# Optimization experiments

Hardware: AMD Instinct MI355X
Metric: run time of the kernel (lower is better)

The kernel has to match this reference:

```python
import jax, jax.numpy as jnp
import numpy as np

SEQ_LENS = np.array([512, 1024, 1536, 2048, 640, 896, 1280, 1792], dtype=np.int64)
T = int(SEQ_LENS.sum())          # 9728 total tokens (cu_seq_len)
D = 2048                          # hidden_size
K = 4                             # kernel_size
GH = 256                          # generator hidden = D // 8


def setup_inputs() -> dict:
    key = jax.random.key(0)
    ks = jax.random.split(key, 6)
    return {
        "x": jax.random.normal(ks[0], (T, D), dtype=jnp.float32),
        "conv_state": jax.random.normal(ks[1], (len(SEQ_LENS), D, K - 1), dtype=jnp.float32),
        "generator_input": jax.random.normal(ks[2], (T, D), dtype=jnp.float32),
        "seq_lens": jnp.asarray(SEQ_LENS),
        "w1": jax.random.normal(ks[3], (D, GH), dtype=jnp.float32) * (1.0 / np.sqrt(D)),
        "w2": jax.random.normal(ks[4], (GH, D * K), dtype=jnp.float32) * (1.0 / np.sqrt(GH)),
        "b2": jax.random.normal(ks[5], (D * K,), dtype=jnp.float32) * 0.01,
    }


def reference(x, conv_state, generator_input, seq_lens, w1, w2, b2):
    lens = np.asarray(seq_lens)              # static ragged lengths
    B = lens.shape[0]
    L = int(lens.max())
    k = conv_state.shape[2] + 1              # kernel_size
    d = x.shape[1]
    t = x.shape[0]

    # ---- kernel generator: Linear -> SiLU -> Linear(+bias), per token ----
    h = jax.nn.silu(generator_input @ w1)                    # (T, GH)
    kern = (h @ w2 + b2).reshape(t, d, k)                    # (T, D, K)

    # ---- left-pad each ragged sequence; prepend conv_state (k-1 steps) ----
    offs = np.concatenate([[0], np.cumsum(lens)])
    x_rows, k_rows = [], []
    for i in range(B):                                        # B is small & static
        xi = jnp.concatenate([conv_state[i].T, x[offs[i]:offs[i + 1]]], axis=0)  # (len_i+k-1, D)
        x_rows.append(jnp.pad(xi, ((L + k - 1 - xi.shape[0], 0), (0, 0))))
        ki = kern[offs[i]:offs[i + 1]]                        # (len_i, D, K)
        k_rows.append(jnp.pad(ki, ((L - int(lens[i]), 0), (0, 0), (0, 0))))
    x_pad = jnp.stack(x_rows)                                 # (B, L+k-1, D)
    k_pad = jnp.stack(k_rows)                                 # (B, L, D, K)

    # new conv state = last k-1 timesteps of the (state+tokens) sequence
    new_conv_state = jnp.swapaxes(x_pad[:, -(k - 1):, :], 1, 2)  # (B, D, k-1)

    # ---- causal dynamic depthwise conv: window j uses x_pad[j:j+k] ----
    out_pad = x_pad[:, 0:L, :] * k_pad[..., 0]
    for kk in range(1, k):                                    # k=4, static tiny loop
        out_pad = out_pad + x_pad[:, kk:kk + L, :] * k_pad[..., kk]  # (B, L, D)

    # ---- un-pad back to ragged layout, apply SiLU ----
    out = jnp.concatenate([out_pad[i, L - int(lens[i]):] for i in range(B)], axis=0)  # (T, D)
    return jax.nn.silu(out), new_conv_state
```

## Files before the change

### kernel.cpp

```cpp
#include <hip/hip_runtime.h>
#include <cstdint>
#include <cstddef>

typedef __attribute__((ext_vector_type(8))) short bf16x8;
typedef __attribute__((ext_vector_type(4))) unsigned short u16x4;
typedef __attribute__((ext_vector_type(4))) unsigned u32x4;
typedef __attribute__((ext_vector_type(4))) float f32x4;
typedef unsigned short u16;

#define T_TOT 9728
#define DDIM  2048
#define GHN   256
#define NSEQ  8

__device__ __constant__ int OFFS[NSEQ + 1] = {0, 512, 1536, 3072, 5120, 5760, 6656, 7936, 9728};

__device__ __forceinline__ u16 f2bf(float f) {
  union { float f; unsigned u; } v; v.f = f;
  unsigned r = v.u + 0x7FFFu + ((v.u >> 16) & 1u);
  return (u16)(r >> 16);
}
__device__ __forceinline__ float silu_f(float v) {
  return v / (1.0f + __expf(-v));
}

__device__ __forceinline__ void pin_reg(bf16x8& v) {
  u32x4& u = reinterpret_cast<u32x4&>(v);
  asm volatile("" : "+v"(u));
}

__device__ __forceinline__ void gload_lds16(const u16* src, u16* dst) {
  __builtin_amdgcn_global_load_lds(
      (__attribute__((address_space(1))) void*)src,
      (__attribute__((address_space(3))) void*)dst,
      16, 0, 0);
}

__global__ __launch_bounds__(256)
void transpose_bf16_k(const float* __restrict__ in, u16* __restrict__ out, int R, int C) {
  __shared__ float tile[64][65];
  const int c0 = blockIdx.x * 64, r0 = blockIdx.y * 64;
  const int tid = threadIdx.x;
  const int lc = tid & 63, lr = tid >> 6;
#pragma unroll
  for (int p = 0; p < 16; ++p) {
    int r = lr + p * 4;
    tile[r][lc] = in[(size_t)(r0 + r) * C + c0 + lc];
  }
  __syncthreads();
#pragma unroll
  for (int p = 0; p < 16; ++p) {
    int c = lr + p * 4;
    out[(size_t)(c0 + c) * R + r0 + lc] = f2bf(tile[lc][c]);
  }
}

__global__ __launch_bounds__(256, 4)
void gemm1_silu(const float* __restrict__ gi, const u16* __restrict__ w1T,
                u16* __restrict__ h) {
  __shared__ u16 A[2][32][72];
  const int tid = threadIdx.x;
  const int lane = tid & 63, wid = tid >> 6;
  const int l15 = lane & 15, l4 = lane >> 4;
  const int t0 = blockIdx.x * 32;
  const int nb = blockIdx.y * 128 + wid * 32;

  f32x4 acc[2][2] = {};

  const int m0 = tid >> 4, f40 = tid & 15;
  const float* g0 = gi + (size_t)(t0 + m0) * DDIM + f40 * 4;
  const float* g1 = gi + (size_t)(t0 + m0 + 16) * DDIM + f40 * 4;

  f32x4 pv0 = *reinterpret_cast<const f32x4*>(g0);
  f32x4 pv1 = *reinterpret_cast<const f32x4*>(g1);

  int p = 0;
  for (int k0 = 0; k0 < DDIM; k0 += 64) {
    u16x4 b0, b1;
    b0[0] = f2bf(pv0[0]); b0[1] = f2bf(pv0[1]); b0[2] = f2bf(pv0[2]); b0[3] = f2bf(pv0[3]);
    b1[0] = f2bf(pv1[0]); b1[1] = f2bf(pv1[1]); b1[2] = f2bf(pv1[2]); b1[3] = f2bf(pv1[3]);
    *reinterpret_cast<u16x4*>(&A[p][m0][f40 * 4]) = b0;
    *reinterpret_cast<u16x4*>(&A[p][m0 + 16][f40 * 4]) = b1;
    if (k0 + 64 < DDIM) {
      pv0 = *reinterpret_cast<const f32x4*>(g0 + k0 + 64);
      pv1 = *reinterpret_cast<const f32x4*>(g1 + k0 + 64);
    }
    __syncthreads();
#pragma unroll
    for (int ks = 0; ks < 2; ++ks) {
      bf16x8 af[2], bfr[2];
#pragma unroll
      for (int mi = 0; mi < 2; ++mi)
        af[mi] = *reinterpret_cast<const bf16x8*>(&A[p][mi * 16 + l15][ks * 32 + 8 * l4]);
#pragma unroll
      for (int ni = 0; ni < 2; ++ni)
        bfr[ni] = *reinterpret_cast<const bf16x8*>(
            &w1T[(size_t)(nb + ni * 16 + l15) * DDIM + k0 + ks * 32 + 8 * l4]);
#pragma unroll
      for (int mi = 0; mi < 2; ++mi)
#pragma unroll
        for (int ni = 0; ni < 2; ++ni)
          acc[mi][ni] = __builtin_amdgcn_mfma_f32_16x16x32_bf16(af[mi], bfr[ni], acc[mi][ni], 0, 0, 0);
    }
    p ^= 1;
  }

#pragma unroll
  for (int mi = 0; mi < 2; ++mi)
#pragma unroll
    for (int ni = 0; ni < 2; ++ni)
#pragma unroll
      for (int r = 0; r < 4; ++r) {
        float v = silu_f(acc[mi][ni][r]);
        int token = t0 + mi * 16 + l4 * 4 + r;
        int c = nb + ni * 16 + l15;
        int pos = ((((c >> 3) ^ (token & 7)) << 3) | (c & 7));
        h[(size_t)token * GHN + pos] = f2bf(v);
      }
}

__global__ __launch_bounds__(256, 2)
void gemm2_conv(const u16* __restrict__ h, const u16* __restrict__ w2T,
                const float* __restrict__ b2, const float* __restrict__ x,
                const float* __restrict__ cs, float* __restrict__ out) {
  __shared__ u16 H[2][64 * 256];
  __shared__ float Ot[64 * 33];
  const int tid = threadIdx.x;
  const int lane = tid & 63, wid = tid >> 6;
  const int l15 = lane & 15, l4 = lane >> 4;
  const int colwave = blockIdx.x * 128 + wid * 32;
  const int d0 = blockIdx.x * 32;
  const int tg = blockIdx.y;

  const int ocol = colwave + 4 * (l15 >> 1) + 2 * (l15 & 1);

  bf16x8 bw[8][2];
#pragma unroll
  for (int ks = 0; ks < 8; ++ks)
#pragma unroll
    for (int ni = 0; ni < 2; ++ni)
      bw[ks][ni] = *reinterpret_cast<const bf16x8*>(
          w2T + (size_t)(ocol + ni) * GHN + ks * 32 + l4 * 8);
#pragma unroll
  for (int ks = 0; ks < 8; ++ks)
#pragma unroll
    for (int ni = 0; ni < 2; ++ni)
      pin_reg(bw[ks][ni]);

  float b2v[2];
#pragma unroll
  for (int ni = 0; ni < 2; ++ni) b2v[ni] = b2[ocol + ni];

  const int d = (colwave >> 2) + (l15 >> 1);
  const int dloc = wid * 8 + (l15 >> 1);
  const int k0t = 2 * (l15 & 1);
  const int par = lane & 1;

  {
    const u16* hb = h + (size_t)(tg * 4) * 64 * GHN;
#pragma unroll
    for (int p = 0; p < 8; ++p)
      gload_lds16(hb + (size_t)(p * 256 + tid) * 8, &H[0][(p * 256 + tid) * 8]);
  }
  __syncthreads();

  int cur = 0;
  for (int it = 0; it < 4; ++it) {
    const int t0 = (tg * 4 + it) * 64;

    if (it < 3) {
      const u16* hb = h + (size_t)(t0 + 64) * GHN;
#pragma unroll
      for (int p = 0; p < 8; ++p)
        gload_lds16(hb + (size_t)(p * 256 + tid) * 8, &H[cur ^ 1][(p * 256 + tid) * 8]);
    }

    int iseq = 0;
    while (OFFS[iseq + 1] <= t0) ++iseq;
    const int seq_start = OFFS[iseq];

    float xw[4][5];
#pragma unroll
    for (int mi = 0; mi < 4; ++mi) {
      const int base = t0 + mi * 16 + l4 * 4;
      const int s0 = base + k0t - 3;
      const float* xr = x + (size_t)s0 * DDIM + d;
      const float* cr = cs + ((size_t)iseq * DDIM + d) * 3 + (s0 - seq_start + 3);
      xw[mi][0] = (s0 >= seq_start) ? xr[0] : cr[0];
      xw[mi][1] = (s0 + 1 >= seq_start) ? xr[DDIM] : cr[1];
      xw[mi][2] = (s0 + 2 >= seq_start) ? xr[2 * DDIM] : cr[2];
      xw[mi][3] = xr[3 * DDIM];
      xw[mi][4] = xr[4 * DDIM];
    }

    f32x4 acc[4][2];
#pragma unroll
    for (int mi = 0; mi < 4; ++mi)
#pragma unroll
      for (int ni = 0; ni < 2; ++ni) {
        acc[mi][ni][0] = b2v[ni]; acc[mi][ni][1] = b2v[ni];
        acc[mi][ni][2] = b2v[ni]; acc[mi][ni][3] = b2v[ni];
      }
    const u16* Hb = H[cur];
#pragma unroll
    for (int ks = 0; ks < 8; ++ks) {
#pragma unroll
      for (int mi = 0; mi < 4; ++mi) {
        int m = mi * 16 + l15;
        int g = ks * 4 + l4;
        bf16x8 af = *reinterpret_cast<const bf16x8*>(&Hb[m * 256 + ((g ^ (m & 7)) << 3)]);
#pragma unroll
        for (int ni = 0; ni < 2; ++ni)
          acc[mi][ni] = __builtin_amdgcn_mfma_f32_16x16x32_bf16(af, bw[ks][ni], acc[mi][ni], 0, 0, 0);
      }
    }

    __syncthreads();

#pragma unroll
    for (int mi = 0; mi < 4; ++mi) {
#pragma unroll
      for (int r = 0; r < 4; ++r) {
        float partial = acc[mi][0][r] * xw[mi][r] + acc[mi][1][r] * xw[mi][r + 1];
        float tot = partial + __shfl_xor(partial, 1);
        if ((r >> 1) == par)
          Ot[(mi * 16 + l4 * 4 + r) * 33 + dloc] = silu_f(tot);
      }
    }

    __syncthreads();

    {
      const int trow = tid >> 2, tq = tid & 3;
      f32x4 o0 = *reinterpret_cast<const f32x4*>(&Ot[trow * 33 + tq * 8]);
      f32x4 o1 = *reinterpret_cast<const f32x4*>(&Ot[trow * 33 + tq * 8 + 4]);
      float* op = out + (size_t)(t0 + trow) * DDIM + d0 + tq * 8;
      *reinterpret_cast<f32x4*>(op) = o0;
      *reinterpret_cast<f32x4*>(op + 4) = o1;
    }
    cur ^= 1;
  }
}

__global__ __launch_bounds__(256)
void tail_state(const float* __restrict__ x, float* __restrict__ out2) {
  int idx = blockIdx.x * 256 + threadIdx.x;
  int i = idx / (DDIM * 3);
  int rem = idx - i * (DDIM * 3);
  int d = rem / 3, m = rem - d * 3;
  int token = OFFS[i + 1] - 3 + m;
  out2[idx] = x[(size_t)token * DDIM + d];
}

extern "C" void kernel_launch(void* const* d_in, const int* in_sizes, int n_in,
                              void* d_out, int out_size, void* d_ws, size_t ws_size,
                              hipStream_t stream) {
  (void)in_sizes; (void)n_in; (void)out_size; (void)ws_size;
  const float* x  = (const float*)d_in[0];
  const float* cs = (const float*)d_in[1];
  const float* gi = (const float*)d_in[2];
  const float* w1 = (const float*)d_in[4];
  const float* w2 = (const float*)d_in[5];
  const float* b2 = (const float*)d_in[6];
  float* out = (float*)d_out;

  char* ws = (char*)d_ws;
  u16* w2T = (u16*)ws;
  u16* w1T = (u16*)(ws + 4194304);
  u16* h   = (u16*)(ws + 4194304 + 1048576);

  transpose_bf16_k<<<dim3(8192 / 64, 256 / 64), 256, 0, stream>>>(w2, w2T, GHN, DDIM * 4);
  transpose_bf16_k<<<dim3(256 / 64, 2048 / 64), 256, 0, stream>>>(w1, w1T, DDIM, GHN);
  gemm1_silu<<<dim3(T_TOT / 32, 2), 256, 0, stream>>>(gi, w1T, h);
  gemm2_conv<<<dim3((DDIM * 4) / 128, T_TOT / 256), 256, 0, stream>>>(h, w2T, b2, x, cs, out);
  tail_state<<<(NSEQ * DDIM * 3) / 256, 256, 0, stream>>>(x, out + (size_t)T_TOT * DDIM);
}
```

Before: 164.2 us.

## Shrink gemm2 token tile, double-buffer output staging, reorder gemm1 grid

gemm2_conv now processes 32-token sub-tiles instead of 64, which halves shared memory and registers per block. It double-buffers the output staging tile so one __syncthreads per iteration can be dropped, and raises the occupancy hint to 3 blocks per CU with twice as many blocks in the grid. gemm1 swaps its grid axes so both column halves of a token tile are adjacent in launch order and reuse the gi rows in cache. Its K loop is also manually unrolled by two with separate prefetch registers. The cost is that each gemm2 block reloads its w2 register fragments for half as many tokens, which doubles total w2 traffic.

```diff
diff --git a/kernel.cpp b/kernel.cpp
--- a/kernel.cpp
+++ b/kernel.cpp
@@ -62,8 +62,8 @@
   const int tid = threadIdx.x;
   const int lane = tid & 63, wid = tid >> 6;
   const int l15 = lane & 15, l4 = lane >> 4;
-  const int t0 = blockIdx.x * 32;
-  const int nb = blockIdx.y * 128 + wid * 32;
+  const int t0 = blockIdx.y * 32;
+  const int nb = blockIdx.x * 128 + wid * 32;
 
   f32x4 acc[2][2] = {};
 
@@ -71,38 +71,68 @@
   const float* g0 = gi + (size_t)(t0 + m0) * DDIM + f40 * 4;
   const float* g1 = gi + (size_t)(t0 + m0 + 16) * DDIM + f40 * 4;
 
-  f32x4 pv0 = *reinterpret_cast<const f32x4*>(g0);
-  f32x4 pv1 = *reinterpret_cast<const f32x4*>(g1);
-
-  int p = 0;
-  for (int k0 = 0; k0 < DDIM; k0 += 64) {
-    u16x4 b0, b1;
-    b0[0] = f2bf(pv0[0]); b0[1] = f2bf(pv0[1]); b0[2] = f2bf(pv0[2]); b0[3] = f2bf(pv0[3]);
-    b1[0] = f2bf(pv1[0]); b1[1] = f2bf(pv1[1]); b1[2] = f2bf(pv1[2]); b1[3] = f2bf(pv1[3]);
-    *reinterpret_cast<u16x4*>(&A[p][m0][f40 * 4]) = b0;
-    *reinterpret_cast<u16x4*>(&A[p][m0 + 16][f40 * 4]) = b1;
-    if (k0 + 64 < DDIM) {
-      pv0 = *reinterpret_cast<const f32x4*>(g0 + k0 + 64);
-      pv1 = *reinterpret_cast<const f32x4*>(g1 + k0 + 64);
-    }
-    __syncthreads();
-#pragma unroll
-    for (int ks = 0; ks < 2; ++ks) {
-      bf16x8 af[2], bfr[2];
-#pragma unroll
-      for (int mi = 0; mi < 2; ++mi)
-        af[mi] = *reinterpret_cast<const bf16x8*>(&A[p][mi * 16 + l15][ks * 32 + 8 * l4]);
-#pragma unroll
-      for (int ni = 0; ni < 2; ++ni)
-        bfr[ni] = *reinterpret_cast<const bf16x8*>(
-            &w1T[(size_t)(nb + ni * 16 + l15) * DDIM + k0 + ks * 32 + 8 * l4]);
-#pragma unroll
-      for (int mi = 0; mi < 2; ++mi)
+  f32x4 pvA0 = *reinterpret_cast<const f32x4*>(g0);
+  f32x4 pvA1 = *reinterpret_cast<const f32x4*>(g1);
+  f32x4 pvB0 = *reinterpret_cast<const f32x4*>(g0 + 64);
+  f32x4 pvB1 = *reinterpret_cast<const f32x4*>(g1 + 64);
+
+  for (int k0 = 0; k0 < DDIM; k0 += 128) {
+    {
+      u16x4 b0, b1;
+      b0[0] = f2bf(pvA0[0]); b0[1] = f2bf(pvA0[1]); b0[2] = f2bf(pvA0[2]); b0[3] = f2bf(pvA0[3]);
+      b1[0] = f2bf(pvA1[0]); b1[1] = f2bf(pvA1[1]); b1[2] = f2bf(pvA1[2]); b1[3] = f2bf(pvA1[3]);
+      *reinterpret_cast<u16x4*>(&A[0][m0][f40 * 4]) = b0;
+      *reinterpret_cast<u16x4*>(&A[0][m0 + 16][f40 * 4]) = b1;
+      if (k0 + 128 < DDIM) {
+        pvA0 = *reinterpret_cast<const f32x4*>(g0 + k0 + 128);
+        pvA1 = *reinterpret_cast<const f32x4*>(g1 + k0 + 128);
+      }
+      __syncthreads();
+#pragma unroll
+      for (int ks = 0; ks < 2; ++ks) {
+        bf16x8 af[2], bfr[2];
+#pragma unroll
+        for (int mi = 0; mi < 2; ++mi)
+          af[mi] = *reinterpret_cast<const bf16x8*>(&A[0][mi * 16 + l15][ks * 32 + 8 * l4]);
 #pragma unroll
         for (int ni = 0; ni < 2; ++ni)
-          acc[mi][ni] = __builtin_amdgcn_mfma_f32_16x16x32_bf16(af[mi], bfr[ni], acc[mi][ni], 0, 0, 0);
-    }
-    p ^= 1;
+          bfr[ni] = *reinterpret_cast<const bf16x8*>(
+              &w1T[(size_t)(nb + ni * 16 + l15) * DDIM + k0 + ks * 32 + 8 * l4]);
+#pragma unroll
+        for (int mi = 0; mi < 2; ++mi)
+#pragma unroll
+          for (int ni = 0; ni < 2; ++ni)
+            acc[mi][ni] = __builtin_amdgcn_mfma_f32_16x16x32_bf16(af[mi], bfr[ni], acc[mi][ni], 0, 0, 0);
+      }
+    }
+    {
+      u16x4 b0, b1;
+      b0[0] = f2bf(pvB0[0]); b0[1] = f2bf(pvB0[1]); b0[2] = f2bf(pvB0[2]); b0[3] = f2bf(pvB0[3]);
+      b1[0] = f2bf(pvB1[0]); b1[1] = f2bf(pvB1[1]); b1[2] = f2bf(pvB1[2]); b1[3] = f2bf(pvB1[3]);
+      *reinterpret_cast<u16x4*>(&A[1][m0][f40 * 4]) = b0;
+      *reinterpret_cast<u16x4*>(&A[1][m0 + 16][f40 * 4]) = b1;
+      if (k0 + 192 < DDIM) {
+        pvB0 = *reinterpret_cast<const f32x4*>(g0 + k0 + 192);
+        pvB1 = *reinterpret_cast<const f32x4*>(g1 + k0 + 192);
+      }
+      __syncthreads();
+#pragma unroll
+      for (int ks = 0; ks < 2; ++ks) {
+        bf16x8 af[2], bfr[2];
+#pragma unroll
+        for (int mi = 0; mi < 2; ++mi)
+          af[mi] = *reinterpret_cast<const bf16x8*>(&A[1][mi * 16 + l15][ks * 32 + 8 * l4]);
+#pragma unroll
+        for (int ni = 0; ni < 2; ++ni)
+          bfr[ni] = *reinterpret_cast<const bf16x8*>(
+              &w1T[(size_t)(nb + ni * 16 + l15) * DDIM + k0 + 64 + ks * 32 + 8 * l4]);
+#pragma unroll
+        for (int mi = 0; mi < 2; ++mi)
+#pragma unroll
+          for (int ni = 0; ni < 2; ++ni)
+            acc[mi][ni] = __builtin_amdgcn_mfma_f32_16x16x32_bf16(af[mi], bfr[ni], acc[mi][ni], 0, 0, 0);
+      }
+    }
   }
 
 #pragma unroll
@@ -119,12 +149,12 @@
       }
 }
 
-__global__ __launch_bounds__(256, 2)
+__global__ __launch_bounds__(256, 3)
 void gemm2_conv(const u16* __restrict__ h, const u16* __restrict__ w2T,
                 const float* __restrict__ b2, const float* __restrict__ x,
                 const float* __restrict__ cs, float* __restrict__ out) {
-  __shared__ u16 H[2][64 * 256];
-  __shared__ float Ot[64 * 33];
+  __shared__ u16 H[2][32 * 256];
+  __shared__ float Ot[2][32 * 33];
   const int tid = threadIdx.x;
   const int lane = tid & 63, wid = tid >> 6;
   const int l15 = lane & 15, l4 = lane >> 4;
@@ -157,21 +187,21 @@
   const int par = lane & 1;
 
   {
-    const u16* hb = h + (size_t)(tg * 4) * 64 * GHN;
-#pragma unroll
-    for (int p = 0; p < 8; ++p)
+    const u16* hb = h + (size_t)(tg * 4) * 32 * GHN;
+#pragma unroll
+    for (int p = 0; p < 4; ++p)
       gload_lds16(hb + (size_t)(p * 256 + tid) * 8, &H[0][(p * 256 + tid) * 8]);
   }
   __syncthreads();
 
-  int cur = 0;
   for (int it = 0; it < 4; ++it) {
-    const int t0 = (tg * 4 + it) * 64;
+    const int t0 = (tg * 4 + it) * 32;
+    const int cur = it & 1;
 
     if (it < 3) {
-      const u16* hb = h + (size_t)(t0 + 64) * GHN;
-#pragma unroll
-      for (int p = 0; p < 8; ++p)
+      const u16* hb = h + (size_t)(t0 + 32) * GHN;
+#pragma unroll
+      for (int p = 0; p < 4; ++p)
         gload_lds16(hb + (size_t)(p * 256 + tid) * 8, &H[cur ^ 1][(p * 256 + tid) * 8]);
     }
 
@@ -179,9 +209,9 @@
     while (OFFS[iseq + 1] <= t0) ++iseq;
     const int seq_start = OFFS[iseq];
 
-    float xw[4][5];
-#pragma unroll
-    for (int mi = 0; mi < 4; ++mi) {
+    float xw[2][5];
+#pragma unroll
+    for (int mi = 0; mi < 2; ++mi) {
       const int base = t0 + mi * 16 + l4 * 4;
       const int s0 = base + k0t - 3;
       const float* xr = x + (size_t)s0 * DDIM + d;
@@ -193,9 +223,9 @@
       xw[mi][4] = xr[4 * DDIM];
     }
 
-    f32x4 acc[4][2];
-#pragma unroll
-    for (int mi = 0; mi < 4; ++mi)
+    f32x4 acc[2][2];
+#pragma unroll
+    for (int mi = 0; mi < 2; ++mi)
 #pragma unroll
       for (int ni = 0; ni < 2; ++ni) {
         acc[mi][ni][0] = b2v[ni]; acc[mi][ni][1] = b2v[ni];
@@ -205,7 +235,7 @@
 #pragma unroll
     for (int ks = 0; ks < 8; ++ks) {
 #pragma unroll
-      for (int mi = 0; mi < 4; ++mi) {
+      for (int mi = 0; mi < 2; ++mi) {
         int m = mi * 16 + l15;
         int g = ks * 4 + l4;
         bf16x8 af = *reinterpret_cast<const bf16x8*>(&Hb[m * 256 + ((g ^ (m & 7)) << 3)]);
@@ -215,30 +245,24 @@
       }
     }
 
-    __syncthreads();
-
-#pragma unroll
-    for (int mi = 0; mi < 4; ++mi) {
+#pragma unroll
+    for (int mi = 0; mi < 2; ++mi) {
 #pragma unroll
       for (int r = 0; r < 4; ++r) {
         float partial = acc[mi][0][r] * xw[mi][r] + acc[mi][1][r] * xw[mi][r + 1];
         float tot = partial + __shfl_xor(partial, 1);
         if ((r >> 1) == par)
-          Ot[(mi * 16 + l4 * 4 + r) * 33 + dloc] = silu_f(tot);
+          Ot[cur][(mi * 16 + l4 * 4 + r) * 33 + dloc] = silu_f(tot);
       }
     }
 
     __syncthreads();
 
     {
-      const int trow = tid >> 2, tq = tid & 3;
-      f32x4 o0 = *reinterpret_cast<const f32x4*>(&Ot[trow * 33 + tq * 8]);
-      f32x4 o1 = *reinterpret_cast<const f32x4*>(&Ot[trow * 33 + tq * 8 + 4]);
-      float* op = out + (size_t)(t0 + trow) * DDIM + d0 + tq * 8;
-      *reinterpret_cast<f32x4*>(op) = o0;
-      *reinterpret_cast<f32x4*>(op + 4) = o1;
-    }
-    cur ^= 1;
+      const int trow = tid >> 3, tq = tid & 7;
+      f32x4 o = *reinterpret_cast<const f32x4*>(&Ot[cur][trow * 33 + tq * 4]);
+      *reinterpret_cast<f32x4*>(out + (size_t)(t0 + trow) * DDIM + d0 + tq * 4) = o;
+    }
   }
 }
 
@@ -271,7 +295,7 @@
 
   transpose_bf16_k<<<dim3(8192 / 64, 256 / 64), 256, 0, stream>>>(w2, w2T, GHN, DDIM * 4);
   transpose_bf16_k<<<dim3(256 / 64, 2048 / 64), 256, 0, stream>>>(w1, w1T, DDIM, GHN);
-  gemm1_silu<<<dim3(T_TOT / 32, 2), 256, 0, stream>>>(gi, w1T, h);
-  gemm2_conv<<<dim3((DDIM * 4) / 128, T_TOT / 256), 256, 0, stream>>>(h, w2T, b2, x, cs, out);
+  gemm1_silu<<<dim3(2, T_TOT / 32), 256, 0, stream>>>(gi, w1T, h);
+  gemm2_conv<<<dim3((DDIM * 4) / 128, T_TOT / 128), 256, 0, stream>>>(h, w2T, b2, x, cs, out);
   tail_state<<<(NSEQ * DDIM * 3) / 256, 256, 0, stream>>>(x, out + (size_t)T_TOT * DDIM);
 }
```

Result: no change. 164.8 us (+0.4%).
